# Performance work log

Measured on AMD Instinct MI355X. Metric: run time of the kernel, lower is better.

The kernel has to match this reference:

```python
import jax, jax.numpy as jnp
from jax import lax
import numpy as np

WIN = 11
SIGMA = 1.5
C1 = 0.01 ** 2  # (K1 * data_range)^2 with data_range=1.0
C2 = 0.03 ** 2


def _gaussian_window(channels: int) -> jnp.ndarray:
    coords = np.arange(WIN, dtype=np.float32) - (WIN - 1) / 2.0
    g = np.exp(-(coords ** 2) / (2.0 * SIGMA ** 2))
    g /= g.sum()
    w2d = np.outer(g, g).astype(np.float32)  # [11,11]
    # OIHW depthwise kernel: [C, 1, 11, 11]
    return jnp.asarray(np.tile(w2d[None, None], (channels, 1, 1, 1)))


def _dwconv(x, w, channels):
    pad = WIN // 2
    return lax.conv_general_dilated(
        x, w, window_strides=(1, 1), padding=[(pad, pad), (pad, pad)],
        dimension_numbers=("NCHW", "OIHW", "NCHW"),
        feature_group_count=channels)


def setup_inputs() -> dict:
    key = jax.random.key(0)
    k1, k2 = jax.random.split(key)
    shape = (16, 3, 512, 512)
    pred = jax.random.uniform(k1, shape, dtype=jnp.float32)
    target = jax.random.uniform(k2, shape, dtype=jnp.float32)
    return {"pred": pred, "target": target}


def reference(pred, target):
    C = pred.shape[1]
    w = _gaussian_window(C).astype(pred.dtype)
    # Stack the five fields along batch so a single depthwise conv computes
    # all local windowed statistics in one pass (fused-stat formulation).
    B = pred.shape[0]
    stacked = jnp.concatenate(
        [pred, target, pred * pred, target * target, pred * target], axis=0)
    stats = _dwconv(stacked, w, C)
    mu1, mu2, e_x2, e_y2, e_xy = (
        stats[0:B], stats[B:2 * B], stats[2 * B:3 * B],
        stats[3 * B:4 * B], stats[4 * B:5 * B])
    mu1_sq = mu1 * mu1
    mu2_sq = mu2 * mu2
    mu1_mu2 = mu1 * mu2
    sigma1_sq = e_x2 - mu1_sq
    sigma2_sq = e_y2 - mu2_sq
    sigma12 = e_xy - mu1_mu2
    ssim_map = ((2.0 * mu1_mu2 + C1) * (2.0 * sigma12 + C2)) / (
        (mu1_sq + mu2_sq + C1) * (sigma1_sq + sigma2_sq + C2))
    return jnp.mean(ssim_map)  # size_average=True
```

## Files before the change

kernel.cpp:

```cpp
#include <hip/hip_runtime.h>
#include <math.h>

#define IMG   512
#define NIMG  48
#define TB    64
#define TC    32
#define SR    74
#define PITCH 77
#define STS   (TC * PITCH)
#define C1v   1.0e-4f
#define C2v   9.0e-4f

struct Win { float w[11]; };

__global__ __launch_bounds__(512, 4) void ssim_kernel(
        const float* __restrict__ pred,
        const float* __restrict__ targ,
        float* __restrict__ partial, Win win) {
    __shared__ float hs[4 * STS];
    __shared__ float wavesum[8];

    const int tid = threadIdx.x;
    const int n   = blockIdx.z;
    const int by  = blockIdx.y;
    const int bx  = blockIdx.x;
    const int y0  = by * TB;
    const int x0  = bx * TC;

    const float* __restrict__ P = pred + (size_t)n * IMG * IMG;
    const float* __restrict__ T = targ + (size_t)n * IMG * IMG;

    #pragma unroll 1
    for (int u = tid; u < SR * 8; u += 512) {
        const int r  = u >> 3;
        const int cb = u & 7;
        const int gy = y0 - 5 + r;
        const bool yok = (gy >= 0) & (gy < IMG);
        const float* __restrict__ Prow = P + (long)gy * IMG;
        const float* __restrict__ Trow = T + (long)gy * IMG;

        float sm[14], dm[14];
        #pragma unroll
        for (int k = 0; k < 5; ++k) {
            const bool zero = (!yok) |
                              ((bx == 0)  & (cb + k <= 1)) |
                              ((bx == 15) & (cb + k >= 10));
            float4 p = make_float4(0.f, 0.f, 0.f, 0.f);
            float4 t = make_float4(0.f, 0.f, 0.f, 0.f);
            if (!zero) {
                const int gx = x0 + 4 * (cb + k - 2);
                p = *(const float4*)(Prow + gx);
                t = *(const float4*)(Trow + gx);
            }
            const float pv[4] = { p.x, p.y, p.z, p.w };
            const float tv[4] = { t.x, t.y, t.z, t.w };
            #pragma unroll
            for (int j = 0; j < 4; ++j) {
                const int w = 4 * k + j;
                if (w >= 3 && w <= 16) {
                    sm[w - 3] = pv[j] + tv[j];
                    dm[w - 3] = pv[j] - tv[j];
                }
            }
        }

        float s1[4], s2[4], q1[4], q2[4];
        #pragma unroll
        for (int i = 0; i < 4; ++i) { s1[i]=0.f; s2[i]=0.f; q1[i]=0.f; q2[i]=0.f; }
        #pragma unroll
        for (int m = 0; m < 14; ++m) {
            const float s  = sm[m];
            const float d  = dm[m];
            const float sq = s * s;
            const float dq = d * d;
            #pragma unroll
            for (int i = 0; i < 4; ++i) {
                const int j = m - i;
                if (j >= 0 && j < 11) {
                    const float wj = win.w[j];
                    s1[i] += wj * s;
                    s2[i] += wj * d;
                    q1[i] += wj * sq;
                    q2[i] += wj * dq;
                }
            }
        }
        const int wbase = (4 * cb) * PITCH + r;
        #pragma unroll
        for (int i = 0; i < 4; ++i) {
            hs[0 * STS + wbase + i * PITCH] = s1[i];
            hs[1 * STS + wbase + i * PITCH] = s2[i];
            hs[2 * STS + wbase + i * PITCH] = q1[i];
            hs[3 * STS + wbase + i * PITCH] = q2[i];
        }
    }
    __syncthreads();

    const int x  = tid & 31;
    const int rg = tid >> 5;
    const int r0 = rg * 4;
    const float* __restrict__ cbase = &hs[x * PITCH + r0];

    float sum[4][4];
    #pragma unroll
    for (int st = 0; st < 4; ++st)
        #pragma unroll
        for (int k = 0; k < 4; ++k) sum[st][k] = 0.f;

    #pragma unroll
    for (int st = 0; st < 4; ++st) {
        float v[14];
        #pragma unroll
        for (int m = 0; m < 14; ++m)
            v[m] = cbase[st * STS + m];
        #pragma unroll
        for (int m = 0; m < 14; ++m) {
            #pragma unroll
            for (int k = 0; k < 4; ++k) {
                if (k >= m - 10 && k <= m)
                    sum[st][k] += win.w[m - k] * v[m];
            }
        }
    }

    float acc = 0.f;
    #pragma unroll
    for (int k = 0; k < 4; ++k) {
        const float S1 = sum[0][k];
        const float S2 = sum[1][k];
        const float Q1 = sum[2][k];
        const float Q2 = sum[3][k];
        const float s1q = S1 * S1;
        const float s2q = S2 * S2;
        const float A_  = 0.5f * (s1q + s2q);
        const float B_  = 0.5f * (s1q - s2q);
        const float sps = 0.5f * (Q1 + Q2) - A_;
        const float sxx = 0.5f * (Q1 - Q2) - B_;
        const float num = (B_ + C1v) * (sxx + C2v);
        const float den = (A_ + C1v) * (sps + C2v);
        acc += num * __builtin_amdgcn_rcpf(den);
    }

    #pragma unroll
    for (int off = 32; off > 0; off >>= 1)
        acc += __shfl_down(acc, off, 64);
    const int wv = tid >> 6;
    if ((tid & 63) == 0) wavesum[wv] = acc;
    __syncthreads();
    if (tid == 0) {
        float s = 0.f;
        #pragma unroll
        for (int i = 0; i < 8; ++i) s += wavesum[i];
        const int bid = (blockIdx.z * gridDim.y + blockIdx.y) * gridDim.x + blockIdx.x;
        partial[bid] = s;
    }
}

__global__ __launch_bounds__(512) void ssim_reduce_kernel(
        const float* __restrict__ partial,
        float* __restrict__ out,
        int nchunk4, double inv_n) {
    __shared__ double wsum[8];
    const float4* __restrict__ p4 = (const float4*)partial;
    double s = 0.0;
    #pragma unroll 1
    for (int i = threadIdx.x; i < nchunk4; i += 512) {
        const float4 v = p4[i];
        s += (double)((v.x + v.y) + (v.z + v.w));
    }
    #pragma unroll
    for (int off = 32; off > 0; off >>= 1)
        s += __shfl_down(s, off, 64);
    const int wv = threadIdx.x >> 6;
    if ((threadIdx.x & 63) == 0) wsum[wv] = s;
    __syncthreads();
    if (threadIdx.x == 0) {
        double tot = 0.0;
        #pragma unroll
        for (int i = 0; i < 8; ++i) tot += wsum[i];
        out[0] = (float)(tot * inv_n);
    }
}

extern "C" void kernel_launch(void* const* d_in, const int* in_sizes, int n_in,
                              void* d_out, int out_size, void* d_ws, size_t ws_size,
                              hipStream_t stream) {
    const float* pred = (const float*)d_in[0];
    const float* targ = (const float*)d_in[1];
    float* out     = (float*)d_out;
    float* partial = (float*)d_ws;

    Win win;
    {
        double v[11], s = 0.0;
        for (int i = 0; i < 11; ++i) {
            float d   = (float)i - 5.0f;
            float arg = -(d * d) / 4.5f;
            v[i] = exp((double)arg);
            s += v[i];
        }
        for (int i = 0; i < 11; ++i) win.w[i] = (float)(v[i] / s);
    }

    dim3 grid(IMG / TC, IMG / TB, NIMG);
    ssim_kernel<<<grid, 512, 0, stream>>>(pred, targ, partial, win);

    const int nblk = (IMG / TC) * (IMG / TB) * NIMG;
    const double inv_n = 1.0 / ((double)NIMG * IMG * IMG);
    ssim_reduce_kernel<<<1, 512, 0, stream>>>(partial, out, nblk / 4, inv_n);
}
```

Before: 61.46 us.

## Specialize interior tiles without bounds guards and raise occupancy target

Splits the horizontal pass into a templated helper, with an unguarded variant for interior tiles so they skip the per-load zero-padding checks. Loads are consumed into the accumulators immediately rather than staged into 14-element arrays, and the vertical pass reads shared memory per tap instead of preloading. Both reduce register pressure, and the launch bound now asks for 8 blocks per CU instead of 4. The risk is register spills under the tighter bound, and code size grows from two instantiations.

```diff
diff --git a/kernel.cpp b/kernel.cpp
--- a/kernel.cpp
+++ b/kernel.cpp
@@ -13,7 +13,71 @@
 
 struct Win { float w[11]; };
 
-__global__ __launch_bounds__(512, 4) void ssim_kernel(
+template<bool GUARD>
+__device__ __forceinline__ void phaseA_unit(
+        float* __restrict__ hs,
+        const float* __restrict__ P,
+        const float* __restrict__ T,
+        const Win& win, int bx, int y0, int x0, int u) {
+    const int r  = u >> 3;
+    const int cb = u & 7;
+    const int gy = y0 - 5 + r;
+    const float* __restrict__ Prow = P + (long)gy * IMG;
+    const float* __restrict__ Trow = T + (long)gy * IMG;
+    const bool yok = (!GUARD) || ((gy >= 0) & (gy < IMG));
+
+    float s1[4], s2[4], q1[4], q2[4];
+    #pragma unroll
+    for (int i = 0; i < 4; ++i) { s1[i]=0.f; s2[i]=0.f; q1[i]=0.f; q2[i]=0.f; }
+
+    #pragma unroll
+    for (int k = 0; k < 5; ++k) {
+        float4 p = make_float4(0.f, 0.f, 0.f, 0.f);
+        float4 t = make_float4(0.f, 0.f, 0.f, 0.f);
+        bool zero = false;
+        if (GUARD)
+            zero = (!yok) | ((bx == 0)  & (cb + k <= 1))
+                          | ((bx == 15) & (cb + k >= 10));
+        if (!zero) {
+            const int gx = x0 + 4 * (cb + k - 2);
+            p = *(const float4*)(Prow + gx);
+            t = *(const float4*)(Trow + gx);
+        }
+        const float pv[4] = { p.x, p.y, p.z, p.w };
+        const float tv[4] = { t.x, t.y, t.z, t.w };
+        #pragma unroll
+        for (int j4 = 0; j4 < 4; ++j4) {
+            const int w = 4 * k + j4;
+            if (w >= 3 && w <= 16) {
+                const float sm = pv[j4] + tv[j4];
+                const float dm = pv[j4] - tv[j4];
+                const float sq = sm * sm;
+                const float dq = dm * dm;
+                #pragma unroll
+                for (int i = 0; i < 4; ++i) {
+                    const int j = w - 3 - i;
+                    if (j >= 0 && j < 11) {
+                        const float wj = win.w[j];
+                        s1[i] += wj * sm;
+                        s2[i] += wj * dm;
+                        q1[i] += wj * sq;
+                        q2[i] += wj * dq;
+                    }
+                }
+            }
+        }
+    }
+    const int wbase = (4 * cb) * PITCH + r;
+    #pragma unroll
+    for (int i = 0; i < 4; ++i) {
+        hs[0 * STS + wbase + i * PITCH] = s1[i];
+        hs[1 * STS + wbase + i * PITCH] = s2[i];
+        hs[2 * STS + wbase + i * PITCH] = q1[i];
+        hs[3 * STS + wbase + i * PITCH] = q2[i];
+    }
+}
+
+__global__ __launch_bounds__(512, 8) void ssim_kernel(
         const float* __restrict__ pred,
         const float* __restrict__ targ,
         float* __restrict__ partial, Win win) {
@@ -30,69 +94,15 @@
     const float* __restrict__ P = pred + (size_t)n * IMG * IMG;
     const float* __restrict__ T = targ + (size_t)n * IMG * IMG;
 
-    #pragma unroll 1
-    for (int u = tid; u < SR * 8; u += 512) {
-        const int r  = u >> 3;
-        const int cb = u & 7;
-        const int gy = y0 - 5 + r;
-        const bool yok = (gy >= 0) & (gy < IMG);
-        const float* __restrict__ Prow = P + (long)gy * IMG;
-        const float* __restrict__ Trow = T + (long)gy * IMG;
-
-        float sm[14], dm[14];
-        #pragma unroll
-        for (int k = 0; k < 5; ++k) {
-            const bool zero = (!yok) |
-                              ((bx == 0)  & (cb + k <= 1)) |
-                              ((bx == 15) & (cb + k >= 10));
-            float4 p = make_float4(0.f, 0.f, 0.f, 0.f);
-            float4 t = make_float4(0.f, 0.f, 0.f, 0.f);
-            if (!zero) {
-                const int gx = x0 + 4 * (cb + k - 2);
-                p = *(const float4*)(Prow + gx);
-                t = *(const float4*)(Trow + gx);
-            }
-            const float pv[4] = { p.x, p.y, p.z, p.w };
-            const float tv[4] = { t.x, t.y, t.z, t.w };
-            #pragma unroll
-            for (int j = 0; j < 4; ++j) {
-                const int w = 4 * k + j;
-                if (w >= 3 && w <= 16) {
-                    sm[w - 3] = pv[j] + tv[j];
-                    dm[w - 3] = pv[j] - tv[j];
-                }
-            }
-        }
-
-        float s1[4], s2[4], q1[4], q2[4];
-        #pragma unroll
-        for (int i = 0; i < 4; ++i) { s1[i]=0.f; s2[i]=0.f; q1[i]=0.f; q2[i]=0.f; }
-        #pragma unroll
-        for (int m = 0; m < 14; ++m) {
-            const float s  = sm[m];
-            const float d  = dm[m];
-            const float sq = s * s;
-            const float dq = d * d;
-            #pragma unroll
-            for (int i = 0; i < 4; ++i) {
-                const int j = m - i;
-                if (j >= 0 && j < 11) {
-                    const float wj = win.w[j];
-                    s1[i] += wj * s;
-                    s2[i] += wj * d;
-                    q1[i] += wj * sq;
-                    q2[i] += wj * dq;
-                }
-            }
-        }
-        const int wbase = (4 * cb) * PITCH + r;
-        #pragma unroll
-        for (int i = 0; i < 4; ++i) {
-            hs[0 * STS + wbase + i * PITCH] = s1[i];
-            hs[1 * STS + wbase + i * PITCH] = s2[i];
-            hs[2 * STS + wbase + i * PITCH] = q1[i];
-            hs[3 * STS + wbase + i * PITCH] = q2[i];
-        }
+    const bool guard = (bx == 0) | (bx == 15) | (by == 0) | (by == (IMG / TB - 1));
+    if (guard) {
+        #pragma unroll 1
+        for (int u = tid; u < SR * 8; u += 512)
+            phaseA_unit<true >(hs, P, T, win, bx, y0, x0, u);
+    } else {
+        #pragma unroll 1
+        for (int u = tid; u < SR * 8; u += 512)
+            phaseA_unit<false>(hs, P, T, win, bx, y0, x0, u);
     }
     __syncthreads();
 
@@ -109,16 +119,15 @@
 
     #pragma unroll
     for (int st = 0; st < 4; ++st) {
-        float v[14];
-        #pragma unroll
-        for (int m = 0; m < 14; ++m)
-            v[m] = cbase[st * STS + m];
+        const float* __restrict__ cp = cbase + st * STS;
         #pragma unroll
         for (int m = 0; m < 14; ++m) {
+            const float v = cp[m];
             #pragma unroll
             for (int k = 0; k < 4; ++k) {
-                if (k >= m - 10 && k <= m)
-                    sum[st][k] += win.w[m - k] * v[m];
+                const int j = m - k;
+                if (j >= 0 && j < 11)
+                    sum[st][k] += win.w[j] * v;
             }
         }
     }
```

Result: faster. 58.43 us (-4.9%).
